# Performance work log

Measured on AMD Instinct MI355X. Metric: run time of the kernel, lower is better.

Reference implementation:

```python
import jax, jax.numpy as jnp
import numpy as np

TOL = 1e-7  # tolerant_zero_error
HID = 32


def _gcn_layer(x, a, W, b):
    # spektral-style GCNConv: relu(A_norm @ X @ W + b)
    return jax.nn.relu(jnp.einsum('bnm,bmf->bnf', a, x @ W) + b)


def setup_inputs() -> dict:
    key = jax.random.key(0)
    ks = jax.random.split(key, 12)
    B, N, F = 8, 2048, 64
    x = jax.random.normal(ks[0], (B, N, F), dtype=jnp.float32)
    a = jax.random.uniform(ks[1], (B, N, N), dtype=jnp.float32)
    def he(k, shape):
        fan_in = shape[0]
        lim = jnp.sqrt(6.0 / fan_in)
        return jax.random.uniform(k, shape, jnp.float32, -lim, lim)
    return {
        'x': x, 'a': a,
        'W1': he(ks[2], (F, HID)),   'b1': jnp.zeros((HID,), jnp.float32),
        'W2': he(ks[3], (HID, HID)), 'b2': jnp.zeros((HID,), jnp.float32),
        'W3': he(ks[4], (HID, HID)), 'b3': jnp.zeros((HID,), jnp.float32),
        'Wf1': he(ks[5], (HID, 2 * HID)), 'bf1': jnp.zeros((2 * HID,), jnp.float32),
        'Wf2': he(ks[6], (2 * HID, 1)),   'bf2': jnp.zeros((1,), jnp.float32),
    }


def reference(x, a, W1, b1, W2, b2, W3, b3, Wf1, bf1, Wf2, bf2):
    x = x.astype(jnp.float32)
    a = a.astype(jnp.float32)
    B, N, _ = a.shape
    # add_self_loop: put 1 on diagonal entries whose current value is ~0
    diag = jnp.diagonal(a, axis1=-2, axis2=-1)            # [B,N]
    add = jnp.where(jnp.abs(diag) < TOL, 1.0, 0.0)        # [B,N]
    eye = jnp.eye(N, dtype=a.dtype)
    a = a + add[:, :, None] * eye
    # norm_a: D^-1/2 A D^-1/2 (diag matmuls == elementwise d_i * a_ij * d_j)
    d = jnp.sum(a, axis=-1)                               # [B,N]
    dm = d ** -0.5
    a = dm[:, :, None] * a * dm[:, None, :]
    # GCNConv stack
    h = _gcn_layer(x, a, W1, b1)
    h = _gcn_layer(h, a, W2, b2)
    h = _gcn_layer(h, a, W3, b3)
    # GlobalMaxPool over nodes
    g = jnp.max(h, axis=1)                                # [B,HID]
    # MLP head
    g = jax.nn.relu(g @ Wf1 + bf1)
    out = g @ Wf2 + bf2                                   # [B,1]
    return out
```

## Files before the change

### kernel.cpp

```cpp
#include <hip/hip_runtime.h>

#define BB 8
#define NN 2048
#define FF 64
#define HH 32
#define CK 128
#define NCHK (NN / CK)

typedef __attribute__((ext_vector_type(8))) short short8;
typedef __attribute__((ext_vector_type(4))) float floatx4;

static __device__ __forceinline__ float warp_sum64(float v) {
  for (int off = 32; off; off >>= 1) v += __shfl_down(v, off, 64);
  return v;
}

static __device__ __forceinline__ float warp_bsum64(float v) {
  for (int off = 1; off < 64; off <<= 1) v += __shfl_xor(v, off, 64);
  return v;
}

static __device__ __forceinline__ unsigned int f2bf_rne(float f) {
  unsigned int u = __float_as_uint(f);
  return (u + 0x7fffu + ((u >> 16) & 1u)) >> 16;
}
static __device__ __forceinline__ float bf2f(unsigned short s) {
  return __uint_as_float(((unsigned int)s) << 16);
}

#define GLOAD_LDS16(g, l)                                                 \
  __builtin_amdgcn_global_load_lds(                                       \
      (const __attribute__((address_space(1))) unsigned int*)(g),         \
      (__attribute__((address_space(3))) unsigned int*)(l), 16, 0, 0)

__global__ __launch_bounds__(256) void deg_cvt_xw_kernel(
    const float* __restrict__ A, const float* __restrict__ x,
    const float* __restrict__ W1, float* __restrict__ dm,
    float* __restrict__ addf, unsigned short* __restrict__ Abf,
    unsigned short* __restrict__ hst, unsigned int* __restrict__ gmax) {
  __shared__ float wl[FF * HH];
  __shared__ float xs[4][FF];
  const int tid = threadIdx.x;
  const int lane = tid & 63;
  const int w = tid >> 6;
  const size_t row = (size_t)blockIdx.x * 4 + w;
  const size_t n = row & (NN - 1);
  const int b = (int)(row >> 11);

  if (blockIdx.x == 0) gmax[tid] = 0;

  for (int k = tid; k < FF * HH; k += 256) wl[k] = W1[k];
  xs[w][lane] = __builtin_nontemporal_load(x + row * FF + lane);

  const float* Ar = A + row * (size_t)NN;
  unsigned int* Abr = (unsigned int*)(Abf + row * (size_t)NN);
  float sum = 0.f;
#pragma unroll
  for (int it = 0; it < 8; ++it) {
    floatx4 v = __builtin_nontemporal_load(
        (const floatx4*)(Ar + it * 256 + lane * 4));
    sum += v.x + v.y + v.z + v.w;
    uint2 p;
    p.x = f2bf_rne(v.x) | (f2bf_rne(v.y) << 16);
    p.y = f2bf_rne(v.z) | (f2bf_rne(v.w) << 16);
    *(uint2*)(Abr + it * 128 + lane * 2) = p;
  }
  sum = warp_bsum64(sum);
  const float diag = Ar[n];
  const float ad = (fabsf(diag) < 1e-7f) ? 1.f : 0.f;
  const float dmv = 1.f / sqrtf(sum + ad);
  if (lane == 0) {
    dm[row] = dmv;
    addf[row] = ad;
  }

  __syncthreads();
  const int c = lane & 31, h = lane >> 5;
  float acc = 0.f;
#pragma unroll
  for (int k = 0; k < 32; ++k) {
    const int kk = h * 32 + k;
    acc = fmaf(xs[w][kk], wl[kk * HH + c], acc);
  }
  acc += __shfl_down(acc, 32, 64);
  if (lane < 32)
    hst[((size_t)b * HH + c) * NN + n] = (unsigned short)f2bf_rne(dmv * acc);
}

__global__ __launch_bounds__(64) void layer_kernel(const unsigned short* __restrict__ Abf,
                                                   const unsigned short* __restrict__ hst_in,
                                                   const float* __restrict__ dm,
                                                   const float* __restrict__ addf,
                                                   const float* __restrict__ bias,
                                                   const float* __restrict__ Wn,
                                                   unsigned short* __restrict__ hst_next,
                                                   unsigned int* __restrict__ gmax,
                                                   const int do_pool) {
  __shared__ __align__(16) unsigned char smem[3][12288];

  const int tid = threadIdx.x;
  const int mb = blockIdx.x & 127;
  const int b = blockIdx.x >> 7;
  const int mrow0 = mb * 16;
  const int q = tid >> 4;
  const int l15 = tid & 15;

  const unsigned short* aSrc[4];
  const unsigned short* bSrc[8];
#pragma unroll
  for (int i = 0; i < 4; ++i) {
    const int r = i * 4 + q;
    const int gl = l15 ^ r;
    aSrc[i] = Abf + ((size_t)(b * NN + mrow0 + r)) * NN + gl * 8;
  }
#pragma unroll
  for (int i = 0; i < 8; ++i) {
    const int r = i * 4 + q;
    const int gl = l15 ^ (r & 15);
    bSrc[i] = hst_in + ((size_t)(b * HH + r)) * NN + gl * 8;
  }

#define ISSUE(buf)                                                        \
  do {                                                                    \
    _Pragma("unroll") for (int i = 0; i < 4; ++i) {                       \
      GLOAD_LDS16(aSrc[i], &smem[buf][i * 1024]);                         \
      aSrc[i] += CK;                                                      \
    }                                                                     \
    _Pragma("unroll") for (int i = 0; i < 8; ++i) {                       \
      GLOAD_LDS16(bSrc[i], &smem[buf][4096 + i * 1024]);                  \
      bSrc[i] += CK;                                                      \
    }                                                                     \
  } while (0)

  floatx4 acc0 = {0.f, 0.f, 0.f, 0.f};
  floatx4 acc1 = {0.f, 0.f, 0.f, 0.f};

  ISSUE(0);
  ISSUE(1);
#pragma unroll
  for (int c = 0; c < NCHK; ++c) {
    if (c + 2 < NCHK) ISSUE((c + 2) % 3);
    if (c <= NCHK - 3) {
      asm volatile("s_waitcnt vmcnt(24)" ::: "memory");
    } else if (c == NCHK - 2) {
      asm volatile("s_waitcnt vmcnt(12)" ::: "memory");
    } else {
      asm volatile("s_waitcnt vmcnt(0)" ::: "memory");
    }
    const unsigned char* Ab = smem[c % 3];
    const unsigned char* Bb = smem[c % 3] + 4096;
#pragma unroll
    for (int ks = 0; ks < 4; ++ks) {
      const int go = (((ks * 4 + q) ^ l15) * 16);
      short8 af = *(const short8*)(Ab + l15 * 256 + go);
      short8 b0 = *(const short8*)(Bb + l15 * 256 + go);
      short8 b1 = *(const short8*)(Bb + 4096 + l15 * 256 + go);
      acc0 = __builtin_amdgcn_mfma_f32_16x16x32_bf16(af, b0, acc0, 0, 0, 0);
      acc1 = __builtin_amdgcn_mfma_f32_16x16x32_bf16(af, b1, acc1, 0, 0, 0);
    }
  }
#undef ISSUE

  const float4 dmq = *(const float4*)(dm + b * NN + mrow0 + q * 4);
  const float4 adq = *(const float4*)(addf + b * NN + mrow0 + q * 4);
  const ushort4 hv0 =
      *(const ushort4*)(hst_in + ((size_t)b * HH + l15) * NN + mrow0 + q * 4);
  const ushort4 hv1 =
      *(const ushort4*)(hst_in + ((size_t)b * HH + 16 + l15) * NN + mrow0 + q * 4);
  float h0[4], h1[4];
#pragma unroll
  for (int r = 0; r < 4; ++r) {
    const float dmv = ((const float*)&dmq)[r];
    const float adv = ((const float*)&adq)[r];
    const float hs0 = bf2f(((const unsigned short*)&hv0)[r]);
    const float hs1 = bf2f(((const unsigned short*)&hv1)[r]);
    h0[r] = fmaxf(fmaf(dmv, acc0[r] + adv * hs0, bias[l15]), 0.f);
    h1[r] = fmaxf(fmaf(dmv, acc1[r] + adv * hs1, bias[16 + l15]), 0.f);
  }

  if (do_pool) {
    float m0 = fmaxf(fmaxf(h0[0], h0[1]), fmaxf(h0[2], h0[3]));
    float m1 = fmaxf(fmaxf(h1[0], h1[1]), fmaxf(h1[2], h1[3]));
    m0 = fmaxf(m0, __shfl_xor(m0, 16, 64));
    m0 = fmaxf(m0, __shfl_xor(m0, 32, 64));
    m1 = fmaxf(m1, __shfl_xor(m1, 16, 64));
    m1 = fmaxf(m1, __shfl_xor(m1, 32, 64));
    if (q == 0) {
      atomicMax(&gmax[b * HH + l15], __float_as_uint(m0));
      atomicMax(&gmax[b * HH + 16 + l15], __float_as_uint(m1));
    }
  } else {
    float* hb = (float*)&smem[0][0];
    __syncthreads();
#pragma unroll
    for (int r = 0; r < 4; ++r) {
      const int row = q * 4 + r;
      hb[row * 33 + l15] = h0[r];
      hb[row * 33 + 16 + l15] = h1[r];
    }
    __syncthreads();
    unsigned short o0[4], o1[4];
#pragma unroll
    for (int r = 0; r < 4; ++r) {
      const int row = q * 4 + r;
      const int rg = b * NN + mrow0 + row;
      float s0 = 0.f, s1 = 0.f;
#pragma unroll
      for (int k = 0; k < HH; ++k) {
        const float hv = hb[row * 33 + k];
        s0 = fmaf(hv, Wn[k * HH + l15], s0);
        s1 = fmaf(hv, Wn[k * HH + 16 + l15], s1);
      }
      const float dmv = dm[rg];
      o0[r] = (unsigned short)f2bf_rne(dmv * s0);
      o1[r] = (unsigned short)f2bf_rne(dmv * s1);
    }
    *(ushort4*)(hst_next + ((size_t)b * HH + l15) * NN + mrow0 + q * 4) =
        *(ushort4*)o0;
    *(ushort4*)(hst_next + ((size_t)b * HH + 16 + l15) * NN + mrow0 + q * 4) =
        *(ushort4*)o1;
  }
}

__global__ __launch_bounds__(64) void head_kernel(const unsigned int* __restrict__ gmax,
                                                  const float* __restrict__ Wf1,
                                                  const float* __restrict__ bf1,
                                                  const float* __restrict__ Wf2,
                                                  const float* __restrict__ bf2,
                                                  float* __restrict__ out) {
  const int b = blockIdx.x;
  const int t = threadIdx.x;
  float acc = bf1[t];
#pragma unroll
  for (int c = 0; c < HH; ++c)
    acc = fmaf(__uint_as_float(gmax[b * HH + c]), Wf1[c * (2 * HH) + t], acc);
  acc = fmaxf(acc, 0.f);
  float v = acc * Wf2[t];
  v = warp_sum64(v);
  if (t == 0) out[b] = v + bf2[0];
}

extern "C" void kernel_launch(void* const* d_in, const int* in_sizes, int n_in,
                              void* d_out, int out_size, void* d_ws, size_t ws_size,
                              hipStream_t stream) {
  const float* x   = (const float*)d_in[0];
  const float* a   = (const float*)d_in[1];
  const float* W1  = (const float*)d_in[2];
  const float* b1  = (const float*)d_in[3];
  const float* W2  = (const float*)d_in[4];
  const float* b2  = (const float*)d_in[5];
  const float* W3  = (const float*)d_in[6];
  const float* b3  = (const float*)d_in[7];
  const float* Wf1 = (const float*)d_in[8];
  const float* bf1 = (const float*)d_in[9];
  const float* Wf2 = (const float*)d_in[10];
  const float* bf2 = (const float*)d_in[11];
  float* out = (float*)d_out;

  float* ws = (float*)d_ws;
  const size_t BN = (size_t)BB * NN;
  float* dm   = ws;
  float* addf = dm + BN;
  unsigned int* gmax = (unsigned int*)(addf + BN);
  unsigned short* hst_a = (unsigned short*)(gmax + 256);
  unsigned short* hst_b = hst_a + BN * HH;
  unsigned short* Abf = hst_b + BN * HH;

  deg_cvt_xw_kernel<<<BN / 4, 256, 0, stream>>>(a, x, W1, dm, addf, Abf, hst_a, gmax);

  layer_kernel<<<BB * 128, 64, 0, stream>>>(Abf, hst_a, dm, addf, b1, W2, hst_b, nullptr, 0);
  layer_kernel<<<BB * 128, 64, 0, stream>>>(Abf, hst_b, dm, addf, b2, W3, hst_a, nullptr, 0);
  layer_kernel<<<BB * 128, 64, 0, stream>>>(Abf, hst_a, dm, addf, b3, nullptr, nullptr, gmax, 1);

  head_kernel<<<BB, 64, 0, stream>>>(gmax, Wf1, bf1, Wf2, bf2, out);
}
```

Measured before the change: 258.1 us.

## Fuse three GCN layers and head into one cooperative kernel with grid syncs

Replaces three layer launches plus the head launch with a single cooperative kernel that runs each layer phase and separates them with grid-wide syncs, then computes the MLP head in block 0. Layer outputs are written with release atomic stores to a third buffer so they are visible across the grid. The aim is to remove kernel launch gaps and tail effects between layers. In exchange it adds grid barrier cost and needs all 1024 blocks co-resident, with a fallback to separate launches if the cooperative launch fails.

```diff
diff --git a/kernel.cpp b/kernel.cpp
--- a/kernel.cpp
+++ b/kernel.cpp
@@ -1,4 +1,7 @@
 #include <hip/hip_runtime.h>
+#include <hip/hip_cooperative_groups.h>
+
+namespace cg = cooperative_groups;
 
 #define BB 8
 #define NN 2048
@@ -87,24 +90,15 @@
     hst[((size_t)b * HH + c) * NN + n] = (unsigned short)f2bf_rne(dmv * acc);
 }
 
-__global__ __launch_bounds__(64) void layer_kernel(const unsigned short* __restrict__ Abf,
-                                                   const unsigned short* __restrict__ hst_in,
-                                                   const float* __restrict__ dm,
-                                                   const float* __restrict__ addf,
-                                                   const float* __restrict__ bias,
-                                                   const float* __restrict__ Wn,
-                                                   unsigned short* __restrict__ hst_next,
-                                                   unsigned int* __restrict__ gmax,
-                                                   const int do_pool) {
-  __shared__ __align__(16) unsigned char smem[3][12288];
-
-  const int tid = threadIdx.x;
-  const int mb = blockIdx.x & 127;
-  const int b = blockIdx.x >> 7;
-  const int mrow0 = mb * 16;
-  const int q = tid >> 4;
-  const int l15 = tid & 15;
-
+static __device__ __forceinline__ void layer_phase(
+    unsigned char (*smem)[12288],
+    const unsigned short* __restrict__ Abf,
+    const unsigned short* __restrict__ hst_in,
+    const float* __restrict__ dm, const float* __restrict__ addf,
+    const float* __restrict__ bias, const float* __restrict__ Wn,
+    unsigned short* __restrict__ hst_next, unsigned int* __restrict__ gmax,
+    const int do_pool, const int b, const int mrow0, const int q,
+    const int l15) {
   const unsigned short* aSrc[4];
   const unsigned short* bSrc[8];
 #pragma unroll
@@ -215,11 +209,78 @@
       o0[r] = (unsigned short)f2bf_rne(dmv * s0);
       o1[r] = (unsigned short)f2bf_rne(dmv * s1);
     }
-    *(ushort4*)(hst_next + ((size_t)b * HH + l15) * NN + mrow0 + q * 4) =
-        *(ushort4*)o0;
-    *(ushort4*)(hst_next + ((size_t)b * HH + 16 + l15) * NN + mrow0 + q * 4) =
-        *(ushort4*)o1;
-  }
+    unsigned long long v0, v1;
+    __builtin_memcpy(&v0, o0, 8);
+    __builtin_memcpy(&v1, o1, 8);
+    __hip_atomic_store(
+        (unsigned long long*)(hst_next + ((size_t)b * HH + l15) * NN + mrow0 + q * 4),
+        v0, __ATOMIC_RELEASE, __HIP_MEMORY_SCOPE_AGENT);
+    __hip_atomic_store(
+        (unsigned long long*)(hst_next + ((size_t)b * HH + 16 + l15) * NN + mrow0 + q * 4),
+        v1, __ATOMIC_RELEASE, __HIP_MEMORY_SCOPE_AGENT);
+  }
+}
+
+__global__ __launch_bounds__(64) void fused_layers_kernel(
+    const unsigned short* __restrict__ Abf,
+    const unsigned short* __restrict__ hst_a,
+    unsigned short* __restrict__ hst_b, unsigned short* __restrict__ hst_c,
+    const float* __restrict__ dm, const float* __restrict__ addf,
+    const float* __restrict__ b1, const float* __restrict__ W2,
+    const float* __restrict__ b2, const float* __restrict__ W3,
+    const float* __restrict__ b3, unsigned int* __restrict__ gmax,
+    const float* __restrict__ Wf1, const float* __restrict__ bf1,
+    const float* __restrict__ Wf2, const float* __restrict__ bf2,
+    float* __restrict__ out) {
+  __shared__ __align__(16) unsigned char smem[3][12288];
+  const int tid = threadIdx.x;
+  const int mb = blockIdx.x & 127;
+  const int b = blockIdx.x >> 7;
+  const int mrow0 = mb * 16;
+  const int q = tid >> 4;
+  const int l15 = tid & 15;
+  cg::grid_group grid = cg::this_grid();
+
+  layer_phase(smem, Abf, hst_a, dm, addf, b1, W2, hst_b, nullptr, 0, b, mrow0,
+              q, l15);
+  grid.sync();
+  layer_phase(smem, Abf, hst_b, dm, addf, b2, W3, hst_c, nullptr, 0, b, mrow0,
+              q, l15);
+  grid.sync();
+  layer_phase(smem, Abf, hst_c, dm, addf, b3, nullptr, nullptr, gmax, 1, b,
+              mrow0, q, l15);
+  grid.sync();
+
+  if (blockIdx.x == 0) {
+#pragma unroll
+    for (int bb = 0; bb < BB; ++bb) {
+      float acc = bf1[tid];
+#pragma unroll
+      for (int c = 0; c < HH; ++c) {
+        const unsigned int gv = __hip_atomic_load(
+            &gmax[bb * HH + c], __ATOMIC_RELAXED, __HIP_MEMORY_SCOPE_AGENT);
+        acc = fmaf(__uint_as_float(gv), Wf1[c * (2 * HH) + tid], acc);
+      }
+      acc = fmaxf(acc, 0.f);
+      float v = acc * Wf2[tid];
+      v = warp_sum64(v);
+      if (tid == 0) out[bb] = v + bf2[0];
+    }
+  }
+}
+
+__global__ __launch_bounds__(64) void layer_kernel(
+    const unsigned short* __restrict__ Abf,
+    const unsigned short* __restrict__ hst_in, const float* __restrict__ dm,
+    const float* __restrict__ addf, const float* __restrict__ bias,
+    const float* __restrict__ Wn, unsigned short* __restrict__ hst_next,
+    unsigned int* __restrict__ gmax, const int do_pool) {
+  __shared__ __align__(16) unsigned char smem[3][12288];
+  const int tid = threadIdx.x;
+  const int mb = blockIdx.x & 127;
+  const int b = blockIdx.x >> 7;
+  layer_phase(smem, Abf, hst_in, dm, addf, bias, Wn, hst_next, gmax, do_pool,
+              b, mb * 16, tid >> 4, tid & 15);
 }
 
 __global__ __launch_bounds__(64) void head_kernel(const unsigned int* __restrict__ gmax,
@@ -264,13 +325,26 @@
   unsigned int* gmax = (unsigned int*)(addf + BN);
   unsigned short* hst_a = (unsigned short*)(gmax + 256);
   unsigned short* hst_b = hst_a + BN * HH;
-  unsigned short* Abf = hst_b + BN * HH;
-
-  deg_cvt_xw_kernel<<<BN / 4, 256, 0, stream>>>(a, x, W1, dm, addf, Abf, hst_a, gmax);
-
-  layer_kernel<<<BB * 128, 64, 0, stream>>>(Abf, hst_a, dm, addf, b1, W2, hst_b, nullptr, 0);
-  layer_kernel<<<BB * 128, 64, 0, stream>>>(Abf, hst_b, dm, addf, b2, W3, hst_a, nullptr, 0);
-  layer_kernel<<<BB * 128, 64, 0, stream>>>(Abf, hst_a, dm, addf, b3, nullptr, nullptr, gmax, 1);
-
-  head_kernel<<<BB, 64, 0, stream>>>(gmax, Wf1, bf1, Wf2, bf2, out);
-}
+  unsigned short* hst_c = hst_b + BN * HH;
+  unsigned short* Abf = hst_c + BN * HH;
+
+  deg_cvt_xw_kernel<<<BN / 4, 256, 0, stream>>>(a, x, W1, dm, addf, Abf, hst_a,
+                                                gmax);
+
+  void* args[] = {&Abf, &hst_a, &hst_b, &hst_c, &dm,  &addf,
+                  &b1,  &W2,    &b2,    &W3,    &b3,  &gmax,
+                  &Wf1, &bf1,   &Wf2,   &bf2,   &out};
+  hipError_t cerr = hipLaunchCooperativeKernel((void*)fused_layers_kernel,
+                                               dim3(BB * 128), dim3(64), args,
+                                               0, stream);
+  if (cerr != hipSuccess) {
+    (void)hipGetLastError();
+    layer_kernel<<<BB * 128, 64, 0, stream>>>(Abf, hst_a, dm, addf, b1, W2,
+                                              hst_b, nullptr, 0);
+    layer_kernel<<<BB * 128, 64, 0, stream>>>(Abf, hst_b, dm, addf, b2, W3,
+                                              hst_c, nullptr, 0);
+    layer_kernel<<<BB * 128, 64, 0, stream>>>(Abf, hst_c, dm, addf, b3,
+                                              nullptr, nullptr, gmax, 1);
+    head_kernel<<<BB, 64, 0, stream>>>(gmax, Wf1, bf1, Wf2, bf2, out);
+  }
+}
```

Result: slower. 618.7 us (+139.7%).
